# Kernel tuning notes

Measured on AMD Instinct MI355X. Metric: run time of the kernel, lower is better.

Reference implementation:

```python
import jax, jax.numpy as jnp
import numpy as np

B, C, H, W = 8, 4, 64, 2048
KH, KW = 3, 5
PH, PW = KH // 2, KW // 2
NUM_ITERS = 3
THETA_GAMMA = 0.9
THETA_ALPHA = 0.9
THETA_BETA = 0.015


def smoothness_kernel(theta):
    # Gaussian over squared window offsets, center zeroed, placed on class diagonal
    hs = jnp.arange(KH, dtype=jnp.float32) - KH // 2
    ws = jnp.arange(KW, dtype=jnp.float32) - KW // 2
    pdist = hs[:, None] ** 2 + ws[None, :] ** 2  # (KH,KW)
    k = jnp.exp(-pdist / (2.0 * theta ** 2))
    k = k.at[KH // 2, KW // 2].set(0.0)
    kernel = jnp.zeros((C, C, KH, KW), jnp.float32)
    kernel = kernel.at[jnp.arange(C), jnp.arange(C)].set(k)
    return kernel


def unfold_neighbors(x):
    # x: (b, c, H, W) -> (b, c, KH*KW-1, H*W), center tap excluded; row-major (kh,kw)
    b, c = x.shape[0], x.shape[1]
    xp = jnp.pad(x, ((0, 0), (0, 0), (PH, PH), (PW, PW)))
    taps = [xp[:, :, dh:dh + H, dw:dw + W]
            for dh in range(KH) for dw in range(KW)]
    K = KH * KW
    del taps[K // 2]  # exclude center pixel
    patches = jnp.stack(taps, axis=2)  # (b, c, K-1, H, W)
    return patches.reshape(b, c, K - 1, H * W)


def conv_same(x, kernel):
    return jax.lax.conv_general_dilated(
        x, kernel, window_strides=(1, 1), padding=[(PH, PH), (PW, PW)],
        dimension_numbers=('NCHW', 'OIHW', 'NCHW'))


def setup_inputs() -> dict:
    key = jax.random.key(0)
    k1, k2, k3 = jax.random.split(key, 3)
    unary = jax.random.normal(k1, (B, C, H, W), jnp.float32)
    xyz = jax.random.normal(k2, (B, 3, H, W), jnp.float32)
    mask = (jax.random.uniform(k3, (B, H, W)) > 0.1).astype(jnp.float32)
    weight_appearance = jnp.ones((1, C, 1, 1), jnp.float32) * 0.1
    weight_smoothness = jnp.ones((1, C, 1, 1), jnp.float32) * 0.02
    compat_w = 1.0 - jnp.eye(C, dtype=jnp.float32)  # Potts label compatibility (O,I)
    return {
        'unary': unary, 'xyz': xyz, 'mask': mask,
        'weight_appearance': weight_appearance,
        'weight_smoothness': weight_smoothness,
        'compat_w': compat_w,
    }


def reference(unary, xyz, mask, weight_appearance, weight_smoothness, compat_w):
    kernel_gamma = smoothness_kernel(THETA_GAMMA)
    kernel_alpha = smoothness_kernel(THETA_ALPHA)
    theta_beta = jnp.full((C,), THETA_BETA, jnp.float32)

    # precompute appearance (bilateral) kernel from xyz; detached in the original
    anchor = xyz.reshape(B, 3, 1, H * W)
    nb = unfold_neighbors(xyz)  # (B,3,14,HW)
    pdist = ((nb - anchor) ** 2).sum(axis=1, keepdims=True)  # (B,1,14,HW)
    kernel_beta = jnp.exp(-pdist / (2.0 * theta_beta[None, :, None, None] ** 2))  # (B,C,14,HW)
    kernel_beta = jax.lax.stop_gradient(kernel_beta)

    m = mask[:, None]  # (B,1,H,W)
    Q = unary
    for _ in range(NUM_ITERS):
        Q = jax.nn.softmax(Q, axis=1)
        k_smooth = conv_same(Q, kernel_gamma)
        # appearance message passing: masked windowed gather weighted by kernel_beta
        masked_Q = Q * m
        Q_nb = unfold_neighbors(masked_Q)  # (B,C,14,HW)
        exp_app = (Q_nb * kernel_beta).sum(axis=2).reshape(B, C, H, W) * m
        exp_smooth = conv_same(Q, kernel_alpha)
        k_app = exp_app * exp_smooth
        weighted_k = weight_smoothness * k_smooth + weight_appearance * k_app
        pairwise = jnp.einsum('oc,bchw->bohw', compat_w, weighted_k)
        Q = unary - pairwise
    return Q
```

## Files before the change

kernel.cpp:

```cpp
#include <hip/hip_runtime.h>
#include <hip/hip_fp16.h>

#define Bsz 8
#define Cn  4
#define Hn  64
#define Wn  2048
#define HW  (Hn*Wn)

#define TW 64
#define TH 8
#define BW 76
#define BH 14
#define NB (BW*BH)
#define R1W 72
#define R1H 12
#define NR1 (R1W*R1H)

#define XBYTES (NB*16)
#define BBYTES (4*NR1*8)

#define G1 0.53940824f
#define G2 0.29096127f
#define G4 0.08465836f
#define G5 0.04566536f

struct Half4 { __half2 lo, hi; };

__device__ __forceinline__ __half hsel(const Half4& h, int k) {
    return (k == 0) ? __low2half(h.lo) : (k == 1) ? __high2half(h.lo)
         : (k == 2) ? __low2half(h.hi) : __high2half(h.hi);
}

__device__ __forceinline__ __half2 GH2(int r, int d) {
    const float Gt[3][5] = {
        {G5, G2, G1, G2, G5},
        {G4, G1, 0.f, G1, G4},
        {G5, G2, G1, G2, G5}};
    return __float2half2_rn(Gt[r][d]);
}

template<bool FINAL>
__device__ __forceinline__ void finish_px(int gh, int gw, int bi,
        __half2 ka, __half2 kb, __half2 aa, __half2 ab, __half mch,
        const float* __restrict__ unary, float* __restrict__ outp,
        Half4* __restrict__ Sout, size_t qbase,
        const float* wa, const float* wsm, const float* cw) {
    bool inimg = (gh >= 0) & (gh < Hn) & (gw >= 0) & (gw < Wn);
    if (inimg) {
        size_t p = (size_t)gh * Wn + gw;
        float ksm[4] = {__low2float(ka), __high2float(ka), __low2float(kb), __high2float(kb)};
        float app[4] = {__low2float(aa), __high2float(aa), __low2float(ab), __high2float(ab)};
        float mc = __half2float(mch);
        float wk[4];
#pragma unroll
        for (int c = 0; c < 4; ++c)
            wk[c] = ksm[c] * (wsm[c] + wa[c] * (app[c] * mc));
        float q[4];
#pragma unroll
        for (int o = 0; o < 4; ++o) {
            float pw = cw[o*4+0]*wk[0] + cw[o*4+1]*wk[1] + cw[o*4+2]*wk[2] + cw[o*4+3]*wk[3];
            q[o] = unary[qbase + p + (size_t)o * HW] - pw;
        }
        if (FINAL) {
#pragma unroll
            for (int o = 0; o < 4; ++o)
                outp[qbase + p + (size_t)o * HW] = q[o];
        } else {
            float mx = fmaxf(fmaxf(q[0], q[1]), fmaxf(q[2], q[3]));
            float e0 = __expf(q[0]-mx), e1 = __expf(q[1]-mx);
            float e2 = __expf(q[2]-mx), e3 = __expf(q[3]-mx);
            float inv = 1.0f / (e0 + e1 + e2 + e3);
            Half4 s; s.lo = __floats2half2_rn(e0*inv, e1*inv);
            s.hi = __floats2half2_rn(e2*inv, e3*inv);
            Sout[bi] = s;
        }
    } else if (!FINAL) {
        Half4 z; z.lo = __float2half2_rn(0.f); z.hi = z.lo;
        Sout[bi] = z;
    }
}

template<int RW, int RH, int OY, int OX, bool FINAL>
__device__ __forceinline__ void do_iter(const Half4* __restrict__ Sin,
                                        Half4* __restrict__ Sout,
                                        const Half4* __restrict__ BETA,
                                        const float* __restrict__ unary,
                                        float* __restrict__ outp,
                                        size_t qbase, int h0, int w0, int tid,
                                        const float* wa, const float* wsm,
                                        const float* cw) {
    constexpr int P = RW * (RH / 2);
    for (int i = tid; i < P; i += 256) {
        int pr = i / RW;
        int pc = i - pr * RW;
        const int r0 = OY + 2 * pr;
        const int c  = OX + pc;
        const int bi0 = (r0 + 3) * BW + (c + 6);
        const int p1  = (r0 + 2) * R1W + (c + 4);

        Half4 B0[4], B1[4];
#pragma unroll
        for (int g = 0; g < 4; ++g) {
            B0[g] = BETA[g * NR1 + p1];
            B1[g] = BETA[g * NR1 + p1 + R1W];
        }

        const __half2 z2 = __float2half2_rn(0.f);
        __half2 k0a = z2, k0b = z2, a0a = z2, a0b = z2;
        __half2 k1a = z2, k1b = z2, a1a = z2, a1b = z2;

#pragma unroll
        for (int j = 0; j < 4; ++j) {
            const int rb = bi0 + (j - 1) * BW;
            Half4 s[5];
#pragma unroll
            for (int d = 0; d < 5; ++d) s[d] = Sin[rb + d - 2];
#pragma unroll
            for (int d = 0; d < 5; ++d) {
                if (j <= 2 && !(j == 1 && d == 2)) {
                    const int t = (j == 0) ? d : (j == 1) ? ((d < 2) ? 5 + d : 4 + d) : 9 + d;
                    const __half2 g2 = GH2(j, d);
                    k0a = __hfma2(g2, s[d].lo, k0a);
                    k0b = __hfma2(g2, s[d].hi, k0b);
                    const __half2 bm2 = __half2half2(hsel(B0[t >> 2], t & 3));
                    a0a = __hfma2(bm2, s[d].lo, a0a);
                    a0b = __hfma2(bm2, s[d].hi, a0b);
                }
                if (j >= 1 && !(j == 2 && d == 2)) {
                    const int t = (j == 1) ? d : (j == 2) ? ((d < 2) ? 5 + d : 4 + d) : 9 + d;
                    const __half2 g2 = GH2(j - 1, d);
                    k1a = __hfma2(g2, s[d].lo, k1a);
                    k1b = __hfma2(g2, s[d].hi, k1b);
                    const __half2 bm2 = __half2half2(hsel(B1[t >> 2], t & 3));
                    a1a = __hfma2(bm2, s[d].lo, a1a);
                    a1b = __hfma2(bm2, s[d].hi, a1b);
                }
            }
        }

        const int gw = w0 + c;
        const int gh0 = h0 + r0;
        finish_px<FINAL>(gh0,     gw, bi0,      k0a, k0b, a0a, a0b, hsel(B0[3], 2),
                         unary, outp, Sout, qbase, wa, wsm, cw);
        finish_px<FINAL>(gh0 + 1, gw, bi0 + BW, k1a, k1b, a1a, a1b, hsel(B1[3], 2),
                         unary, outp, Sout, qbase, wa, wsm, cw);
    }
}

__global__ __launch_bounds__(256, 3) void crf_fused(const float* __restrict__ unary,
                                                    const float* __restrict__ xyz,
                                                    const float* __restrict__ mask,
                                                    const float* __restrict__ wa_g,
                                                    const float* __restrict__ wsm_g,
                                                    const float* __restrict__ cw_g,
                                                    float* __restrict__ outp) {
    __shared__ __align__(16) unsigned char LDS_[XBYTES + BBYTES];
    Half4*  SA   = (Half4*)LDS_;
    Half4*  SB   = SA + NB;
    float4* XBUF = (float4*)LDS_;
    Half4*  BETA = (Half4*)(LDS_ + XBYTES);

    const int tid = threadIdx.x;
    const int w0 = blockIdx.x * TW;
    const int h0 = blockIdx.y * TH;
    const int b  = blockIdx.z;

    const size_t qbase = (size_t)b * Cn * HW;
    const size_t xbase = (size_t)b * 3 * HW;
    const size_t mbase = (size_t)b * HW;

    float wa[4], wsm[4], cw[16];
#pragma unroll
    for (int k = 0; k < 4; ++k) { wa[k] = wa_g[k]; wsm[k] = wsm_g[k]; }
#pragma unroll
    for (int k = 0; k < 16; ++k) cw[k] = cw_g[k];

    for (int i = tid; i < NB; i += 256) {
        int br = i / BW, bc = i - br * BW;
        int gh = h0 + br - 3, gw = w0 + bc - 6;
        float4 xm = make_float4(0.f, 0.f, 0.f, 0.f);
        if (gh >= 0 && gh < Hn && gw >= 0 && gw < Wn) {
            size_t p = (size_t)gh * Wn + gw;
            xm = make_float4(xyz[xbase + p], xyz[xbase + p + HW],
                             xyz[xbase + p + 2 * HW], mask[mbase + p]);
        }
        XBUF[i] = xm;
    }
    __syncthreads();

    for (int p = tid; p < NR1; p += 256) {
        int r1 = p / R1W, c1 = p - r1 * R1W;
        int bi = (r1 + 1) * BW + (c1 + 2);
        float4 xc = XBUF[bi];
        float bm[14];
        int t = 0;
#pragma unroll
        for (int dh = -1; dh <= 1; ++dh) {
#pragma unroll
            for (int dw = -2; dw <= 2; ++dw) {
                if (dh == 0 && dw == 0) continue;
                float4 xn = XBUF[bi + dh * BW + dw];
                float dx = xn.x - xc.x, dy = xn.y - xc.y, dz = xn.z - xc.z;
                bm[t++] = __expf(-2222.2222f * (dx*dx + dy*dy + dz*dz)) * xn.w;
            }
        }
        Half4 g0, g1, g2, g3;
        g0.lo = __floats2half2_rn(bm[0],  bm[1]);  g0.hi = __floats2half2_rn(bm[2],  bm[3]);
        g1.lo = __floats2half2_rn(bm[4],  bm[5]);  g1.hi = __floats2half2_rn(bm[6],  bm[7]);
        g2.lo = __floats2half2_rn(bm[8],  bm[9]);  g2.hi = __floats2half2_rn(bm[10], bm[11]);
        g3.lo = __floats2half2_rn(bm[12], bm[13]); g3.hi = __floats2half2_rn(xc.w, 0.f);
        BETA[0 * NR1 + p] = g0; BETA[1 * NR1 + p] = g1;
        BETA[2 * NR1 + p] = g2; BETA[3 * NR1 + p] = g3;
    }
    __syncthreads();

    for (int i = tid; i < NB; i += 256) {
        int br = i / BW, bc = i - br * BW;
        int gh = h0 + br - 3, gw = w0 + bc - 6;
        Half4 s; s.lo = __float2half2_rn(0.f); s.hi = s.lo;
        if (gh >= 0 && gh < Hn && gw >= 0 && gw < Wn) {
            size_t p = (size_t)gh * Wn + gw;
            float q0 = unary[qbase + p];
            float q1 = unary[qbase + p + HW];
            float q2 = unary[qbase + p + 2 * HW];
            float q3 = unary[qbase + p + 3 * HW];
            float mx = fmaxf(fmaxf(q0, q1), fmaxf(q2, q3));
            float e0 = __expf(q0 - mx), e1 = __expf(q1 - mx);
            float e2 = __expf(q2 - mx), e3 = __expf(q3 - mx);
            float inv = 1.0f / (e0 + e1 + e2 + e3);
            s.lo = __floats2half2_rn(e0 * inv, e1 * inv);
            s.hi = __floats2half2_rn(e2 * inv, e3 * inv);
        }
        SA[i] = s;
    }
    __syncthreads();

    do_iter<R1W, R1H, -2, -4, false>(SA, SB, BETA, unary, nullptr, qbase, h0, w0, tid, wa, wsm, cw);
    __syncthreads();
    do_iter<68, 10, -1, -2, false>(SB, SA, BETA, unary, nullptr, qbase, h0, w0, tid, wa, wsm, cw);
    __syncthreads();
    do_iter<64, 8, 0, 0, true>(SA, nullptr, BETA, unary, outp, qbase, h0, w0, tid, wa, wsm, cw);
}

extern "C" void kernel_launch(void* const* d_in, const int* in_sizes, int n_in,
                              void* d_out, int out_size, void* d_ws, size_t ws_size,
                              hipStream_t stream) {
    const float* unary  = (const float*)d_in[0];
    const float* xyz    = (const float*)d_in[1];
    const float* mask   = (const float*)d_in[2];
    const float* wa     = (const float*)d_in[3];
    const float* wsm    = (const float*)d_in[4];
    const float* compat = (const float*)d_in[5];
    float* outp = (float*)d_out;

    dim3 grid(Wn / TW, Hn / TH, Bsz), blk(256);
    crf_fused<<<grid, blk, 0, stream>>>(unary, xyz, mask, wa, wsm, compat, outp);
}
```

Before: 123.4 us.

## Keep bilateral weights in registers, enlarge tiles, use fixed work region per iter

The appearance (beta) weights now live in per-thread registers, each thread owning one or two fixed pixel pairs, instead of an LDS table. That frees LDS so the tile can double in height (16 rows, 512 threads), which reduces the fraction of halo recomputation across the three fused mean-field iterations. Every iteration now computes over the full 72x20 region rather than a shrinking one, so some work is wasted in later iterations, and the larger per-thread register state risks lower occupancy.

```diff
diff --git a/kernel.cpp b/kernel.cpp
--- a/kernel.cpp
+++ b/kernel.cpp
@@ -8,16 +8,14 @@
 #define HW  (Hn*Wn)
 
 #define TW 64
-#define TH 8
+#define TH 16
+#define BLK 512
 #define BW 76
-#define BH 14
+#define BH 22
 #define NB (BW*BH)
 #define R1W 72
-#define R1H 12
-#define NR1 (R1W*R1H)
-
-#define XBYTES (NB*16)
-#define BBYTES (4*NR1*8)
+#define R1H 20
+#define NP1 (R1W*(R1H/2))
 
 #define G1 0.53940824f
 #define G2 0.29096127f
@@ -25,32 +23,57 @@
 #define G5 0.04566536f
 
 struct Half4 { __half2 lo, hi; };
-
-__device__ __forceinline__ __half hsel(const Half4& h, int k) {
-    return (k == 0) ? __low2half(h.lo) : (k == 1) ? __high2half(h.lo)
-         : (k == 2) ? __low2half(h.hi) : __high2half(h.hi);
-}
-
-__device__ __forceinline__ __half2 GH2(int r, int d) {
-    const float Gt[3][5] = {
-        {G5, G2, G1, G2, G5},
-        {G4, G1, 0.f, G1, G4},
-        {G5, G2, G1, G2, G5}};
-    return __float2half2_rn(Gt[r][d]);
+struct Beta { __half2 t[14]; __half2 mk; };
+
+__device__ __forceinline__ float Gw(int r, int d) {
+    const float Gt[3][5] = {{G5,G2,G1,G2,G5},{G4,G1,0.f,G1,G4},{G5,G2,G1,G2,G5}};
+    return Gt[r][d];
+}
+__device__ __forceinline__ constexpr int tap_of(int r, int d) {
+    return (r == 0) ? d : (r == 1) ? ((d < 2) ? 5 + d : 4 + d) : 9 + d;
+}
+
+__device__ __forceinline__ void compute_beta(int pair, const float4* __restrict__ X,
+                                             Beta& B) {
+    const int pr = pair / R1W;
+    const int pc = pair - pr * R1W;
+    const int bx0 = (2 * pr + 1) * BW + pc + 2;
+    const float4 xc0 = X[bx0];
+    const float4 xc1 = X[bx0 + BW];
+    float bm0[14], bm1[14];
+#pragma unroll
+    for (int j = 0; j < 4; ++j) {
+        const int rb = bx0 + (j - 1) * BW;
+#pragma unroll
+        for (int d = 0; d < 5; ++d) {
+            const float4 xn = X[rb + d - 2];
+            if (j <= 2 && !(j == 1 && d == 2)) {
+                float dx = xn.x - xc0.x, dy = xn.y - xc0.y, dz = xn.z - xc0.z;
+                bm0[tap_of(j, d)] = __expf(-2222.2222f * (dx*dx + dy*dy + dz*dz)) * xn.w;
+            }
+            if (j >= 1 && !(j == 2 && d == 2)) {
+                float dx = xn.x - xc1.x, dy = xn.y - xc1.y, dz = xn.z - xc1.z;
+                bm1[tap_of(j - 1, d)] = __expf(-2222.2222f * (dx*dx + dy*dy + dz*dz)) * xn.w;
+            }
+        }
+    }
+#pragma unroll
+    for (int t = 0; t < 14; ++t) B.t[t] = __floats2half2_rn(bm0[t], bm1[t]);
+    B.mk = __floats2half2_rn(xc0.w, xc1.w);
 }
 
 template<bool FINAL>
-__device__ __forceinline__ void finish_px(int gh, int gw, int bi,
-        __half2 ka, __half2 kb, __half2 aa, __half2 ab, __half mch,
+__device__ __forceinline__ void finish_one(int gh, int gw, int bi,
+        __half2 ka, __half2 kb, __half2 aa, __half2 ab, float mc,
         const float* __restrict__ unary, float* __restrict__ outp,
         Half4* __restrict__ Sout, size_t qbase,
-        const float* wa, const float* wsm, const float* cw) {
-    bool inimg = (gh >= 0) & (gh < Hn) & (gw >= 0) & (gw < Wn);
+        const float* wa, const float* wsm, const float* cw, bool store_ok) {
+    if (FINAL && !store_ok) return;
+    const bool inimg = FINAL || ((gh >= 0) & (gh < Hn) & (gw >= 0) & (gw < Wn));
     if (inimg) {
         size_t p = (size_t)gh * Wn + gw;
         float ksm[4] = {__low2float(ka), __high2float(ka), __low2float(kb), __high2float(kb)};
         float app[4] = {__low2float(aa), __high2float(aa), __low2float(ab), __high2float(ab)};
-        float mc = __half2float(mch);
         float wk[4];
 #pragma unroll
         for (int c = 0; c < 4; ++c)
@@ -80,85 +103,68 @@
     }
 }
 
-template<int RW, int RH, int OY, int OX, bool FINAL>
-__device__ __forceinline__ void do_iter(const Half4* __restrict__ Sin,
-                                        Half4* __restrict__ Sout,
-                                        const Half4* __restrict__ BETA,
-                                        const float* __restrict__ unary,
-                                        float* __restrict__ outp,
-                                        size_t qbase, int h0, int w0, int tid,
-                                        const float* wa, const float* wsm,
-                                        const float* cw) {
-    constexpr int P = RW * (RH / 2);
-    for (int i = tid; i < P; i += 256) {
-        int pr = i / RW;
-        int pc = i - pr * RW;
-        const int r0 = OY + 2 * pr;
-        const int c  = OX + pc;
-        const int bi0 = (r0 + 3) * BW + (c + 6);
-        const int p1  = (r0 + 2) * R1W + (c + 4);
-
-        Half4 B0[4], B1[4];
-#pragma unroll
-        for (int g = 0; g < 4; ++g) {
-            B0[g] = BETA[g * NR1 + p1];
-            B1[g] = BETA[g * NR1 + p1 + R1W];
-        }
-
-        const __half2 z2 = __float2half2_rn(0.f);
-        __half2 k0a = z2, k0b = z2, a0a = z2, a0b = z2;
-        __half2 k1a = z2, k1b = z2, a1a = z2, a1b = z2;
-
-#pragma unroll
-        for (int j = 0; j < 4; ++j) {
-            const int rb = bi0 + (j - 1) * BW;
-            Half4 s[5];
-#pragma unroll
-            for (int d = 0; d < 5; ++d) s[d] = Sin[rb + d - 2];
-#pragma unroll
-            for (int d = 0; d < 5; ++d) {
-                if (j <= 2 && !(j == 1 && d == 2)) {
-                    const int t = (j == 0) ? d : (j == 1) ? ((d < 2) ? 5 + d : 4 + d) : 9 + d;
-                    const __half2 g2 = GH2(j, d);
-                    k0a = __hfma2(g2, s[d].lo, k0a);
-                    k0b = __hfma2(g2, s[d].hi, k0b);
-                    const __half2 bm2 = __half2half2(hsel(B0[t >> 2], t & 3));
-                    a0a = __hfma2(bm2, s[d].lo, a0a);
-                    a0b = __hfma2(bm2, s[d].hi, a0b);
-                }
-                if (j >= 1 && !(j == 2 && d == 2)) {
-                    const int t = (j == 1) ? d : (j == 2) ? ((d < 2) ? 5 + d : 4 + d) : 9 + d;
-                    const __half2 g2 = GH2(j - 1, d);
-                    k1a = __hfma2(g2, s[d].lo, k1a);
-                    k1b = __hfma2(g2, s[d].hi, k1b);
-                    const __half2 bm2 = __half2half2(hsel(B1[t >> 2], t & 3));
-                    a1a = __hfma2(bm2, s[d].lo, a1a);
-                    a1b = __hfma2(bm2, s[d].hi, a1b);
-                }
-            }
-        }
-
-        const int gw = w0 + c;
-        const int gh0 = h0 + r0;
-        finish_px<FINAL>(gh0,     gw, bi0,      k0a, k0b, a0a, a0b, hsel(B0[3], 2),
-                         unary, outp, Sout, qbase, wa, wsm, cw);
-        finish_px<FINAL>(gh0 + 1, gw, bi0 + BW, k1a, k1b, a1a, a1b, hsel(B1[3], 2),
-                         unary, outp, Sout, qbase, wa, wsm, cw);
-    }
-}
-
-__global__ __launch_bounds__(256, 3) void crf_fused(const float* __restrict__ unary,
+template<bool FINAL>
+__device__ __forceinline__ void do_pair(int pair, const Half4* __restrict__ Sin,
+        Half4* __restrict__ Sout, const Beta& B,
+        const float* __restrict__ unary, float* __restrict__ outp,
+        size_t qbase, int h0, int w0,
+        const float* wa, const float* wsm, const float* cw) {
+    const int pr = pair / R1W;
+    const int pc = pair - pr * R1W;
+    const int bx0 = (2 * pr + 1) * BW + pc + 2;
+
+    const __half2 z2 = __float2half2_rn(0.f);
+    __half2 k0a=z2,k0b=z2,a0a=z2,a0b=z2,k1a=z2,k1b=z2,a1a=z2,a1b=z2;
+
+#pragma unroll
+    for (int j = 0; j < 4; ++j) {
+        const int rb = bx0 + (j - 1) * BW;
+        Half4 s[5];
+#pragma unroll
+        for (int d = 0; d < 5; ++d) s[d] = Sin[rb + d - 2];
+#pragma unroll
+        for (int d = 0; d < 5; ++d) {
+            if (j <= 2 && !(j == 1 && d == 2)) {
+                const int t = tap_of(j, d);
+                const __half2 g2 = __float2half2_rn(Gw(j, d));
+                k0a = __hfma2(g2, s[d].lo, k0a);
+                k0b = __hfma2(g2, s[d].hi, k0b);
+                const __half2 bm2 = __half2half2(__low2half(B.t[t]));
+                a0a = __hfma2(bm2, s[d].lo, a0a);
+                a0b = __hfma2(bm2, s[d].hi, a0b);
+            }
+            if (j >= 1 && !(j == 2 && d == 2)) {
+                const int t = tap_of(j - 1, d);
+                const __half2 g2 = __float2half2_rn(Gw(j - 1, d));
+                k1a = __hfma2(g2, s[d].lo, k1a);
+                k1b = __hfma2(g2, s[d].hi, k1b);
+                const __half2 bm2 = __half2half2(__high2half(B.t[t]));
+                a1a = __hfma2(bm2, s[d].lo, a1a);
+                a1b = __hfma2(bm2, s[d].hi, a1b);
+            }
+        }
+    }
+
+    const int gw = w0 + pc - 4;
+    const int gh0 = h0 + 2 * pr - 2;
+    const bool ok = (pr >= 1) & (pr <= 8) & (pc >= 4) & (pc <= 67);
+    finish_one<FINAL>(gh0,     gw, bx0,      k0a, k0b, a0a, a0b, __low2float(B.mk),
+                      unary, outp, Sout, qbase, wa, wsm, cw, ok);
+    finish_one<FINAL>(gh0 + 1, gw, bx0 + BW, k1a, k1b, a1a, a1b, __high2float(B.mk),
+                      unary, outp, Sout, qbase, wa, wsm, cw, ok);
+}
+
+__global__ __launch_bounds__(BLK, 4) void crf_fused(const float* __restrict__ unary,
                                                     const float* __restrict__ xyz,
                                                     const float* __restrict__ mask,
                                                     const float* __restrict__ wa_g,
                                                     const float* __restrict__ wsm_g,
                                                     const float* __restrict__ cw_g,
                                                     float* __restrict__ outp) {
-    __shared__ __align__(16) unsigned char LDS_[XBYTES + BBYTES];
+    __shared__ __align__(16) unsigned char LDS_[NB * 16];
     Half4*  SA   = (Half4*)LDS_;
-    Half4*  SB   = SA + NB;
+    Half4*  SB   = (Half4*)(LDS_ + NB * 8);
     float4* XBUF = (float4*)LDS_;
-    Half4*  BETA = (Half4*)(LDS_ + XBYTES);
 
     const int tid = threadIdx.x;
     const int w0 = blockIdx.x * TW;
@@ -175,7 +181,7 @@
 #pragma unroll
     for (int k = 0; k < 16; ++k) cw[k] = cw_g[k];
 
-    for (int i = tid; i < NB; i += 256) {
+    for (int i = tid; i < NB; i += BLK) {
         int br = i / BW, bc = i - br * BW;
         int gh = h0 + br - 3, gw = w0 + bc - 6;
         float4 xm = make_float4(0.f, 0.f, 0.f, 0.f);
@@ -188,33 +194,13 @@
     }
     __syncthreads();
 
-    for (int p = tid; p < NR1; p += 256) {
-        int r1 = p / R1W, c1 = p - r1 * R1W;
-        int bi = (r1 + 1) * BW + (c1 + 2);
-        float4 xc = XBUF[bi];
-        float bm[14];
-        int t = 0;
-#pragma unroll
-        for (int dh = -1; dh <= 1; ++dh) {
-#pragma unroll
-            for (int dw = -2; dw <= 2; ++dw) {
-                if (dh == 0 && dw == 0) continue;
-                float4 xn = XBUF[bi + dh * BW + dw];
-                float dx = xn.x - xc.x, dy = xn.y - xc.y, dz = xn.z - xc.z;
-                bm[t++] = __expf(-2222.2222f * (dx*dx + dy*dy + dz*dz)) * xn.w;
-            }
-        }
-        Half4 g0, g1, g2, g3;
-        g0.lo = __floats2half2_rn(bm[0],  bm[1]);  g0.hi = __floats2half2_rn(bm[2],  bm[3]);
-        g1.lo = __floats2half2_rn(bm[4],  bm[5]);  g1.hi = __floats2half2_rn(bm[6],  bm[7]);
-        g2.lo = __floats2half2_rn(bm[8],  bm[9]);  g2.hi = __floats2half2_rn(bm[10], bm[11]);
-        g3.lo = __floats2half2_rn(bm[12], bm[13]); g3.hi = __floats2half2_rn(xc.w, 0.f);
-        BETA[0 * NR1 + p] = g0; BETA[1 * NR1 + p] = g1;
-        BETA[2 * NR1 + p] = g2; BETA[3 * NR1 + p] = g3;
-    }
-    __syncthreads();
-
-    for (int i = tid; i < NB; i += 256) {
+    Beta B0, B1;
+    compute_beta(tid, XBUF, B0);
+    const bool t2 = tid < (NP1 - BLK);
+    if (t2) compute_beta(tid + BLK, XBUF, B1);
+    __syncthreads();
+
+    for (int i = tid; i < NB; i += BLK) {
         int br = i / BW, bc = i - br * BW;
         int gh = h0 + br - 3, gw = w0 + bc - 6;
         Half4 s; s.lo = __float2half2_rn(0.f); s.hi = s.lo;
@@ -232,14 +218,19 @@
             s.hi = __floats2half2_rn(e2 * inv, e3 * inv);
         }
         SA[i] = s;
-    }
-    __syncthreads();
-
-    do_iter<R1W, R1H, -2, -4, false>(SA, SB, BETA, unary, nullptr, qbase, h0, w0, tid, wa, wsm, cw);
-    __syncthreads();
-    do_iter<68, 10, -1, -2, false>(SB, SA, BETA, unary, nullptr, qbase, h0, w0, tid, wa, wsm, cw);
-    __syncthreads();
-    do_iter<64, 8, 0, 0, true>(SA, nullptr, BETA, unary, outp, qbase, h0, w0, tid, wa, wsm, cw);
+        Half4 z; z.lo = __float2half2_rn(0.f); z.hi = z.lo;
+        SB[i] = z;
+    }
+    __syncthreads();
+
+    do_pair<false>(tid, SA, SB, B0, unary, nullptr, qbase, h0, w0, wa, wsm, cw);
+    if (t2) do_pair<false>(tid + BLK, SA, SB, B1, unary, nullptr, qbase, h0, w0, wa, wsm, cw);
+    __syncthreads();
+    do_pair<false>(tid, SB, SA, B0, unary, nullptr, qbase, h0, w0, wa, wsm, cw);
+    if (t2) do_pair<false>(tid + BLK, SB, SA, B1, unary, nullptr, qbase, h0, w0, wa, wsm, cw);
+    __syncthreads();
+    do_pair<true>(tid, SA, nullptr, B0, unary, outp, qbase, h0, w0, wa, wsm, cw);
+    if (t2) do_pair<true>(tid + BLK, SA, nullptr, B1, unary, outp, qbase, h0, w0, wa, wsm, cw);
 }
 
 extern "C" void kernel_launch(void* const* d_in, const int* in_sizes, int n_in,
@@ -253,6 +244,6 @@
     const float* compat = (const float*)d_in[5];
     float* outp = (float*)d_out;
 
-    dim3 grid(Wn / TW, Hn / TH, Bsz), blk(256);
+    dim3 grid(Wn / TW, Hn / TH, Bsz), blk(BLK);
     crf_fused<<<grid, blk, 0, stream>>>(unary, xyz, mask, wa, wsm, compat, outp);
 }
```

After: 145.3 us. 1.18x slower.
